# Optimization experiments

Measured on AMD Instinct MI355X. Metric: run time of the kernel, lower is better.

## Reference

```python
import jax, jax.numpy as jnp
import numpy as np
from jax import lax

B, N, H, W, C = 8, 1024, 256, 256, 256
HID = 512
RATES = (1, 3, 9, 9, 3, 1)


def setup_inputs() -> dict:
    key = jax.random.key(0)
    ks = jax.random.split(key, 16)
    # vertices are (row, col) float coordinates inside the feature map
    vertices = jax.random.uniform(ks[0], (B, N, 2), jnp.float32) * jnp.array([H - 1, W - 1], jnp.float32)
    features = jax.random.normal(ks[1], (B, H, W, C), jnp.float32)
    inp = {"vertices": vertices, "features": features}
    # Conv1D stack params (haiku Conv1D: kernel [K, Cin, Cout], bias [Cout])
    cin = C
    for i in range(6):
        inp[f"w{i}"] = jax.random.normal(ks[2 + 2 * i], (3, cin, HID), jnp.float32) * 0.05
        inp[f"b{i}"] = jax.random.normal(ks[3 + 2 * i], (HID,), jnp.float32) * 0.05
        cin = HID
    # offset head: Conv1D(2, 1, with_bias=False); original zero-init, randomized here
    inp["w_off"] = jax.random.normal(ks[14], (1, HID, 2), jnp.float32) * 0.05
    return inp


def _conv1d(x, w, b, rate):
    # x: [B, N, Cin], w: [K, Cin, Cout] -> SAME-padded dilated conv over vertex axis
    y = lax.conv_general_dilated(x, w, window_strides=(1,), padding="SAME",
                                 rhs_dilation=(rate,),
                                 dimension_numbers=("NWC", "WIO", "NWC"))
    return y if b is None else y + b


def _sample_at_vertices(vertices, features):
    # bilinear interpolation, zero outside (map_coordinates order=1 mode='constant')
    Bb, Hh, Ww, Cc = features.shape
    y, x = vertices[..., 0], vertices[..., 1]  # [B, N]
    y0f, x0f = jnp.floor(y), jnp.floor(x)
    wy1, wx1 = y - y0f, x - x0f
    wy0, wx0 = 1.0 - wy1, 1.0 - wx1
    y0, x0 = y0f.astype(jnp.int32), x0f.astype(jnp.int32)
    flat = features.reshape(Bb, Hh * Ww, Cc)

    def gather(yi, xi, wgt):
        valid = (yi >= 0) & (yi < Hh) & (xi >= 0) & (xi < Ww)
        idx = jnp.clip(yi, 0, Hh - 1) * Ww + jnp.clip(xi, 0, Ww - 1)  # [B, N]
        vals = jnp.take_along_axis(flat, idx[..., None], axis=1)  # [B, N, C]
        return vals * (wgt * valid)[..., None]

    return (gather(y0, x0, wy0 * wx0) + gather(y0, x0 + 1, wy0 * wx1)
            + gather(y0 + 1, x0, wy1 * wx0) + gather(y0 + 1, x0 + 1, wy1 * wx1))


def reference(vertices, features, w0, b0, w1, b1, w2, b2, w3, b3, w4, b4, w5, b5, w_off):
    h = _sample_at_vertices(vertices, features)  # [B, N, C]
    ws = (w0, w1, w2, w3, w4, w5)
    bs = (b0, b1, b2, b3, b4, b5)
    for w, b, r in zip(ws, bs, RATES):
        h = jax.nn.relu(_conv1d(h, w, b, r))
    offsets = _conv1d(h, w_off, None, 1)  # [B, N, 2]
    return vertices + offsets
```

## Files before the change

### kernel.cpp

```cpp
#include <hip/hip_runtime.h>

#define BATCH 8
#define NPTS  1024
#define FH    256
#define FW    256
#define FC    256
#define HID   512
#define PADN  1056
#define HALO  16

typedef __attribute__((ext_vector_type(8))) short short8;
typedef __attribute__((ext_vector_type(16))) float f32x16;
typedef unsigned short ushort_t;
typedef unsigned int uint_t;

__device__ __forceinline__ ushort_t f2bf(float f) {
    uint_t u = __builtin_bit_cast(uint_t, f);
    u += 0x7fffu + ((u >> 16) & 1u);
    return (ushort_t)(u >> 16);
}
__device__ __forceinline__ float bf2f(ushort_t s) {
    uint_t u = ((uint_t)s) << 16;
    return __builtin_bit_cast(float, u);
}

#define GLOAD16(g, l)                                                     \
    __builtin_amdgcn_global_load_lds(                                     \
        (const __attribute__((address_space(1))) void*)(g),               \
        (__attribute__((address_space(3))) void*)(l), 16, 0, 0)

__device__ __forceinline__ short8 gread16(const short* p) {
    short8 r;
    asm volatile("global_load_dwordx4 %0, %1, off" : "=v"(r) : "v"(p));
    return r;
}

__global__ __launch_bounds__(256) void prep_kernel(
    const float* __restrict__ vertices, const float* __restrict__ features,
    const float* __restrict__ w0, const float* __restrict__ w1,
    const float* __restrict__ w2, const float* __restrict__ w3,
    const float* __restrict__ w4, const float* __restrict__ w5,
    ushort_t* __restrict__ wt0, ushort_t* __restrict__ wt1,
    ushort_t* __restrict__ wt2, ushort_t* __restrict__ wt3,
    ushort_t* __restrict__ wt4, ushort_t* __restrict__ wt5,
    ushort_t* __restrict__ XpA, ushort_t* __restrict__ XpB,
    ushort_t* __restrict__ XpC, float* __restrict__ out)
{
    __shared__ float tile[64][65];
    const int blk = blockIdx.x;
    const int tid = threadIdx.x;

    if (blk < 1280) {
        int i = blk * 256 + tid;
        if (i < 65536) {
            int b = i >> 13, rem = i & 8191;
            int strip = rem >> 12, off = rem & 4095;
            XpA[(size_t)b * (PADN * FC) + (strip ? (PADN - HALO) * FC : 0) + off] = 0;
        }
        int jB = i - 65536;
        if (jB >= 0 && jB < 262144) {
            ushort_t* T = (jB < 131072) ? XpB : XpC;
            int j = jB & 131071;
            int b = j >> 14, rem = j & 16383;
            int strip = rem >> 13, off = rem & 8191;
            T[(size_t)b * (PADN * HID) + (strip ? (PADN - HALO) * HID : 0) + off] = 0;
        }
        return;
    }

    if (blk < 2336) {
        int j = blk - 1280;
        const float* w; ushort_t* wt; int CIN, kk0, co0;
        if (j < 96) {
            w = w0; wt = wt0; CIN = FC;
            kk0 = (j % 12) * 64; co0 = (j / 12) * 64;
        } else {
            int j2 = j - 96;
            int layer = j2 / 192, jj = j2 % 192;
            const float* ws[5]  = {w1, w2, w3, w4, w5};
            ushort_t*   wts[5]  = {wt1, wt2, wt3, wt4, wt5};
            w = ws[layer]; wt = wts[layer]; CIN = HID;
            kk0 = (jj % 24) * 64; co0 = (jj / 24) * 64;
        }
        int tap = kk0 / CIN, ci0 = kk0 - tap * CIN;
        int SL  = (3 * CIN) >> 4;
#pragma unroll 4
        for (int it = 0; it < 16; ++it) {
            int r = it * 4 + (tid >> 6);
            tile[r][tid & 63] = w[((size_t)tap * CIN + ci0 + r) * HID + co0 + (tid & 63)];
        }
        __syncthreads();
        int gl  = tid >> 7;
        int r2  = tid & 127;
        int l   = r2 >> 1;
        int j0  = (r2 & 1) * 4;
        int gco = (co0 >> 5) + gl;
        int kb  = ((l >> 5) << 3);
        int cl  = gl * 32 + (l & 31);
#pragma unroll
        for (int si = 0; si < 4; ++si) {
            int s = (kk0 >> 4) + si;
            ushort4 v;
            v.x = f2bf(tile[si * 16 + kb + j0 + 0][cl]);
            v.y = f2bf(tile[si * 16 + kb + j0 + 1][cl]);
            v.z = f2bf(tile[si * 16 + kb + j0 + 2][cl]);
            v.w = f2bf(tile[si * 16 + kb + j0 + 3][cl]);
            *(ushort4*)(wt + ((((size_t)gco * SL) + s) << 9) + l * 8 + j0) = v;
        }
        return;
    }

    if (blk < 4384) {
        int p = (blk - 2336) * 4 + (tid >> 6);
        int b = p >> 10;
        int n = p & 1023;
        int t = tid & 63;

        float y = vertices[2 * p + 0];
        float x = vertices[2 * p + 1];
        float y0f = floorf(y), x0f = floorf(x);
        float wy1 = y - y0f, wx1 = x - x0f;
        float wy0 = 1.f - wy1, wx0 = 1.f - wx1;
        int y0 = (int)y0f, x0 = (int)x0f;

        float4 acc = make_float4(0.f, 0.f, 0.f, 0.f);
        const float4* fbase = (const float4*)features + (size_t)b * FH * FW * (FC / 4);

#define CORNER(yi, xi, wgt) {                                                  \
        int yy = (yi), xx = (xi);                                              \
        float wv = ((yy >= 0) && (yy < FH) && (xx >= 0) && (xx < FW)) ? (wgt) : 0.f; \
        int yc = yy < 0 ? 0 : (yy > FH - 1 ? FH - 1 : yy);                     \
        int xc = xx < 0 ? 0 : (xx > FW - 1 ? FW - 1 : xx);                     \
        float4 v = fbase[((size_t)yc * FW + xc) * (FC / 4) + t];               \
        acc.x += v.x * wv; acc.y += v.y * wv; acc.z += v.z * wv; acc.w += v.w * wv; }

        CORNER(y0,     x0,     wy0 * wx0);
        CORNER(y0,     x0 + 1, wy0 * wx1);
        CORNER(y0 + 1, x0,     wy1 * wx0);
        CORNER(y0 + 1, x0 + 1, wy1 * wx1);
#undef CORNER

        ushort4 o;
        o.x = f2bf(acc.x); o.y = f2bf(acc.y); o.z = f2bf(acc.z); o.w = f2bf(acc.w);
        *(ushort4*)(XpA + ((size_t)b * PADN + HALO + n) * FC + 4 * t) = o;
        return;
    }

    {
        int i = (blk - 4384) * 256 + tid;
        out[i] = vertices[i];
    }
}

template <int CIN, bool HEAD>
__global__ __launch_bounds__(512, 2) void conv_mfma(
    const ushort_t* __restrict__ Xp,
    const ushort_t* __restrict__ Wf,
    const float* __restrict__ bias,
    ushort_t* __restrict__ Yp,
    int rate,
    const float* __restrict__ w_off,
    float* __restrict__ out)
{
    constexpr int NC  = CIN / 64;
    constexpr int SL3 = CIN / 16;
    constexpr int SL  = 3 * SL3;
    __shared__ short lds[2][18432];

    const int tid  = threadIdx.x;
    const int wid  = tid >> 6;
    const int lane = tid & 63;
    const int wm   = wid >> 2;
    const int wk   = wid & 3;

    const int h  = blockIdx.x;
    const int bm = (h & 7) * 4 + (h >> 6);
    const int bn = (h >> 3) & 7;
    const int batch = bm >> 2;
    const int n0    = (bm & 3) * 256;
    const int co0   = bn * 64;

    const short* Xbase = (const short*)Xp + ((size_t)batch * PADN + n0) * CIN;
    const short* Wbase = (const short*)Wf + lane * 8;

    auto stageA = [&](int buf, int c) {
        const short* Ag = Xbase + c * 64;
        short* ldsA = &lds[buf][0];
#pragma unroll
        for (int it = 0; it < 4; ++it) {
            int slot = it * 512 + wid * 64 + lane;
            int row  = slot >> 3;
            int chnk = (slot & 7) ^ (row & 7);
            GLOAD16(Ag + (size_t)row * CIN + chnk * 8,
                    ldsA + (size_t)(it * 512 + wid * 64) * 8);
        }
        if (wid < 4) {
            int slot = 2048 + wid * 64 + lane;
            int row  = slot >> 3;
            int chnk = (slot & 7) ^ (row & 7);
            GLOAD16(Ag + (size_t)row * CIN + chnk * 8,
                    ldsA + (size_t)(2048 + wid * 64) * 8);
        }
    };
    auto loadB = [&](short8* dst, int c) {
#pragma unroll
        for (int t = 0; t < 3; ++t)
#pragma unroll
            for (int j = 0; j < 2; ++j) {
                size_t gco = (size_t)(bn * 2 + j);
                size_t sl  = (size_t)(t * SL3 + c * 4 + wk);
                dst[t * 2 + j] = gread16(Wbase + ((gco * SL + sl) << 9));
            }
    };

    f32x16 acc[4][2];
    const int rowA0 = wm * 128 + (lane & 31);
    {
        float bv0 = (wk == 0) ? bias[co0 + (lane & 31)] : 0.f;
        float bv1 = (wk == 0) ? bias[co0 + 32 + (lane & 31)] : 0.f;
#pragma unroll
        for (int i = 0; i < 4; ++i)
#pragma unroll
            for (int r = 0; r < 16; ++r) { acc[i][0][r] = bv0; acc[i][1][r] = bv1; }
    }

    short8 B0[6], B1[6];
    stageA(0, 0);
    __builtin_amdgcn_sched_barrier(0);
    loadB(B0, 0);
    __builtin_amdgcn_sched_barrier(0);
    asm volatile("s_waitcnt vmcnt(6)" ::: "memory");
    __builtin_amdgcn_s_barrier();
    __builtin_amdgcn_sched_barrier(0);

    int cur = 0;
    auto kstep = [&](int c, short8* Bcur, short8* Bnxt) {
        if (c + 1 < NC) stageA(cur ^ 1, c + 1);
        __builtin_amdgcn_sched_barrier(0);

        if (c + 1 < NC) asm volatile("s_waitcnt vmcnt(4)" ::: "memory");
        else            asm volatile("s_waitcnt vmcnt(0)" ::: "memory");
        __builtin_amdgcn_sched_barrier(0);

        const short* As = &lds[cur][0];
        const int ch = wk * 2 + (lane >> 5);
        __builtin_amdgcn_s_setprio(1);
#pragma unroll
        for (int t = 0; t < 3; ++t) {
            const int shift = 16 + (t - 1) * rate;
#pragma unroll
            for (int i = 0; i < 4; ++i) {
                int rr = rowA0 + i * 32 + shift;
                short8 av = *(const short8*)(As + rr * 64 + ((ch ^ (rr & 7)) << 3));
                acc[i][0] = __builtin_amdgcn_mfma_f32_32x32x16_bf16(
                    av, Bcur[t * 2 + 0], acc[i][0], 0, 0, 0);
                acc[i][1] = __builtin_amdgcn_mfma_f32_32x32x16_bf16(
                    av, Bcur[t * 2 + 1], acc[i][1], 0, 0, 0);
            }
        }
        __builtin_amdgcn_s_setprio(0);
        __builtin_amdgcn_sched_barrier(0);

        if (c + 1 < NC) {
            loadB(Bnxt, c + 1);
            __builtin_amdgcn_sched_barrier(0);
            asm volatile("s_waitcnt vmcnt(6)" ::: "memory");
        }
        __builtin_amdgcn_s_barrier();
        cur ^= 1;
    };

    for (int c = 0; c < NC; c += 2) {
        kstep(c,     B0, B1);
        kstep(c + 1, B1, B0);
    }

    float* pf = (float*)&lds[0][0];
#pragma unroll
    for (int p = 1; p < 4; ++p) {
        if (wk == p) {
#pragma unroll
            for (int i = 0; i < 4; ++i)
#pragma unroll
                for (int j = 0; j < 2; ++j)
#pragma unroll
                    for (int r = 0; r < 16; ++r)
                        pf[wm * 8192 + ((i * 2 + j) * 16 + r) * 64 + lane] = acc[i][j][r];
        }
        __syncthreads();
        if (wk == 0) {
#pragma unroll
            for (int i = 0; i < 4; ++i)
#pragma unroll
                for (int j = 0; j < 2; ++j)
#pragma unroll
                    for (int r = 0; r < 16; ++r)
                        acc[i][j][r] += pf[wm * 8192 + ((i * 2 + j) * 16 + r) * 64 + lane];
        }
        __syncthreads();
    }

    if (wk == 0) {
        if (!HEAD) {
            ushort_t* Yb = Yp + ((size_t)batch * PADN + HALO + n0) * HID + co0;
#pragma unroll
            for (int i = 0; i < 4; ++i) {
#pragma unroll
                for (int r = 0; r < 16; ++r) {
                    int rrow = wm * 128 + i * 32 + (r & 3) + 8 * (r >> 2) + 4 * (lane >> 5);
#pragma unroll
                    for (int j = 0; j < 2; ++j) {
                        float v = acc[i][j][r];
                        v = v > 0.f ? v : 0.f;
                        Yb[(size_t)rrow * HID + j * 32 + (lane & 31)] = f2bf(v);
                    }
                }
            }
        } else {
            const int col = lane & 31;
            float w00 = w_off[(co0 + col) * 2 + 0];
            float w01 = w_off[(co0 + col) * 2 + 1];
            float w10 = w_off[(co0 + 32 + col) * 2 + 0];
            float w11 = w_off[(co0 + 32 + col) * 2 + 1];
#pragma unroll
            for (int i = 0; i < 4; ++i) {
#pragma unroll
                for (int r = 0; r < 16; ++r) {
                    float v0 = acc[i][0][r]; v0 = v0 > 0.f ? v0 : 0.f;
                    float v1 = acc[i][1][r]; v1 = v1 > 0.f ? v1 : 0.f;
                    float s0 = v0 * w00 + v1 * w10;
                    float s1 = v0 * w01 + v1 * w11;
#pragma unroll
                    for (int m = 16; m >= 1; m >>= 1) {
                        s0 += __shfl_xor(s0, m);
                        s1 += __shfl_xor(s1, m);
                    }
                    if (col == 0) {
                        int row = n0 + wm * 128 + i * 32 + (r & 3) + 8 * (r >> 2) + 4 * (lane >> 5);
                        float* op = out + 2 * ((size_t)batch * NPTS + row);
                        atomicAdd(op + 0, s0);
                        atomicAdd(op + 1, s1);
                    }
                }
            }
        }
    }
}

extern "C" void kernel_launch(void* const* d_in, const int* in_sizes, int n_in,
                              void* d_out, int out_size, void* d_ws, size_t ws_size,
                              hipStream_t stream)
{
    (void)in_sizes; (void)n_in; (void)out_size; (void)ws_size;

    const float* vertices = (const float*)d_in[0];
    const float* features = (const float*)d_in[1];
    const float* w[6]  = {(const float*)d_in[2], (const float*)d_in[4],
                          (const float*)d_in[6], (const float*)d_in[8],
                          (const float*)d_in[10], (const float*)d_in[12]};
    const float* bb[6] = {(const float*)d_in[3], (const float*)d_in[5],
                          (const float*)d_in[7], (const float*)d_in[9],
                          (const float*)d_in[11], (const float*)d_in[13]};
    const float* w_off = (const float*)d_in[14];
    float* out = (float*)d_out;

    char* p = (char*)d_ws;
    ushort_t* wt[6];
    wt[0] = (ushort_t*)p; p += (size_t)HID * (3 * FC) * 2;
    for (int i = 1; i < 6; ++i) { wt[i] = (ushort_t*)p; p += (size_t)HID * (3 * HID) * 2; }
    ushort_t* XpA = (ushort_t*)p; p += (size_t)BATCH * PADN * FC  * 2;
    ushort_t* XpB = (ushort_t*)p; p += (size_t)BATCH * PADN * HID * 2;
    ushort_t* XpC = (ushort_t*)p;

    prep_kernel<<<4448, 256, 0, stream>>>(
        vertices, features, w[0], w[1], w[2], w[3], w[4], w[5],
        wt[0], wt[1], wt[2], wt[3], wt[4], wt[5], XpA, XpB, XpC, out);

    static const int rates[6] = {1, 3, 9, 9, 3, 1};
    conv_mfma<FC, false><<<256, 512, 0, stream>>>(
        XpA, wt[0], bb[0], XpB, rates[0], nullptr, nullptr);
    ushort_t* src = XpB;
    ushort_t* dst = XpC;
    for (int i = 1; i < 5; ++i) {
        conv_mfma<HID, false><<<256, 512, 0, stream>>>(
            src, wt[i], bb[i], dst, rates[i], nullptr, nullptr);
        ushort_t* tmp = src; src = dst; dst = tmp;
    }
    conv_mfma<HID, true><<<256, 512, 0, stream>>>(
        src, wt[5], bb[5], dst, rates[5], w_off, out);
}
```

Baseline: 142.4 us.

## Split warps over output columns and K halves to shrink split-K reduction

Result: faster. 124.1 us (-12.9%).

```diff
diff --git a/kernel.cpp b/kernel.cpp
--- a/kernel.cpp
+++ b/kernel.cpp
@@ -171,7 +171,8 @@
     const int wid  = tid >> 6;
     const int lane = tid & 63;
     const int wm   = wid >> 2;
-    const int wk   = wid & 3;
+    const int wn   = (wid >> 1) & 1;
+    const int wk   = wid & 1;
 
     const int h  = blockIdx.x;
     const int bm = (h & 7) * 4 + (h >> 6);
@@ -181,7 +182,8 @@
     const int co0   = bn * 64;
 
     const short* Xbase = (const short*)Xp + ((size_t)batch * PADN + n0) * CIN;
-    const short* Wbase = (const short*)Wf + lane * 8;
+    const short* Wb = (const short*)Wf
+                    + (((size_t)(bn * 2 + wn) * SL) << 9) + lane * 8;
 
     auto stageA = [&](int buf, int c) {
         const short* Ag = Xbase + c * 64;
@@ -206,22 +208,20 @@
 #pragma unroll
         for (int t = 0; t < 3; ++t)
 #pragma unroll
-            for (int j = 0; j < 2; ++j) {
-                size_t gco = (size_t)(bn * 2 + j);
-                size_t sl  = (size_t)(t * SL3 + c * 4 + wk);
-                dst[t * 2 + j] = gread16(Wbase + ((gco * SL + sl) << 9));
-            }
+            for (int ksh = 0; ksh < 2; ++ksh)
+                dst[t * 2 + ksh] =
+                    gread16(Wb + ((size_t)(t * SL3 + c * 4 + wk * 2 + ksh) << 9));
     };
 
-    f32x16 acc[4][2];
+    f32x16 acc[4];
     const int rowA0 = wm * 128 + (lane & 31);
+    const int coB   = wn * 32 + (lane & 31);
     {
-        float bv0 = (wk == 0) ? bias[co0 + (lane & 31)] : 0.f;
-        float bv1 = (wk == 0) ? bias[co0 + 32 + (lane & 31)] : 0.f;
+        float bv = (wk == 0) ? bias[co0 + coB] : 0.f;
 #pragma unroll
         for (int i = 0; i < 4; ++i)
 #pragma unroll
-            for (int r = 0; r < 16; ++r) { acc[i][0][r] = bv0; acc[i][1][r] = bv1; }
+            for (int r = 0; r < 16; ++r) acc[i][r] = bv;
     }
 
     short8 B0[6], B1[6];
@@ -243,19 +243,20 @@
         __builtin_amdgcn_sched_barrier(0);
 
         const short* As = &lds[cur][0];
-        const int ch = wk * 2 + (lane >> 5);
         __builtin_amdgcn_s_setprio(1);
 #pragma unroll
         for (int t = 0; t < 3; ++t) {
             const int shift = 16 + (t - 1) * rate;
 #pragma unroll
-            for (int i = 0; i < 4; ++i) {
-                int rr = rowA0 + i * 32 + shift;
-                short8 av = *(const short8*)(As + rr * 64 + ((ch ^ (rr & 7)) << 3));
-                acc[i][0] = __builtin_amdgcn_mfma_f32_32x32x16_bf16(
-                    av, Bcur[t * 2 + 0], acc[i][0], 0, 0, 0);
-                acc[i][1] = __builtin_amdgcn_mfma_f32_32x32x16_bf16(
-                    av, Bcur[t * 2 + 1], acc[i][1], 0, 0, 0);
+            for (int ksh = 0; ksh < 2; ++ksh) {
+                int ch = (wk * 2 + ksh) * 2 + (lane >> 5);
+#pragma unroll
+                for (int i = 0; i < 4; ++i) {
+                    int rr = rowA0 + i * 32 + shift;
+                    short8 av = *(const short8*)(As + rr * 64 + ((ch ^ (rr & 7)) << 3));
+                    acc[i] = __builtin_amdgcn_mfma_f32_32x32x16_bf16(
+                        av, Bcur[t * 2 + ksh], acc[i], 0, 0, 0);
+                }
             }
         }
         __builtin_amdgcn_s_setprio(0);
@@ -276,30 +277,15 @@
     }
 
     float* pf = (float*)&lds[0][0];
-#pragma unroll
-    for (int p = 1; p < 4; ++p) {
-        if (wk == p) {
-#pragma unroll
-            for (int i = 0; i < 4; ++i)
-#pragma unroll
-                for (int j = 0; j < 2; ++j)
-#pragma unroll
-                    for (int r = 0; r < 16; ++r)
-                        pf[wm * 8192 + ((i * 2 + j) * 16 + r) * 64 + lane] = acc[i][j][r];
-        }
-        __syncthreads();
-        if (wk == 0) {
-#pragma unroll
-            for (int i = 0; i < 4; ++i)
-#pragma unroll
-                for (int j = 0; j < 2; ++j)
-#pragma unroll
-                    for (int r = 0; r < 16; ++r)
-                        acc[i][j][r] += pf[wm * 8192 + ((i * 2 + j) * 16 + r) * 64 + lane];
-        }
-        __syncthreads();
-    }
-
+    const int pair = wm * 2 + wn;
+    if (wk == 1) {
+#pragma unroll
+        for (int i = 0; i < 4; ++i)
+#pragma unroll
+            for (int r = 0; r < 16; ++r)
+                pf[pair * 4096 + (i * 16 + r) * 64 + lane] = acc[i][r];
+    }
+    __syncthreads();
     if (wk == 0) {
         if (!HEAD) {
             ushort_t* Yb = Yp + ((size_t)batch * PADN + HALO + n0) * HID + co0;
@@ -308,34 +294,28 @@
 #pragma unroll
                 for (int r = 0; r < 16; ++r) {
                     int rrow = wm * 128 + i * 32 + (r & 3) + 8 * (r >> 2) + 4 * (lane >> 5);
-#pragma unroll
-                    for (int j = 0; j < 2; ++j) {
-                        float v = acc[i][j][r];
-                        v = v > 0.f ? v : 0.f;
-                        Yb[(size_t)rrow * HID + j * 32 + (lane & 31)] = f2bf(v);
-                    }
+                    float v = acc[i][r] + pf[pair * 4096 + (i * 16 + r) * 64 + lane];
+                    v = v > 0.f ? v : 0.f;
+                    Yb[(size_t)rrow * HID + coB] = f2bf(v);
                 }
             }
         } else {
-            const int col = lane & 31;
-            float w00 = w_off[(co0 + col) * 2 + 0];
-            float w01 = w_off[(co0 + col) * 2 + 1];
-            float w10 = w_off[(co0 + 32 + col) * 2 + 0];
-            float w11 = w_off[(co0 + 32 + col) * 2 + 1];
+            float wc0 = w_off[(co0 + coB) * 2 + 0];
+            float wc1 = w_off[(co0 + coB) * 2 + 1];
 #pragma unroll
             for (int i = 0; i < 4; ++i) {
 #pragma unroll
                 for (int r = 0; r < 16; ++r) {
-                    float v0 = acc[i][0][r]; v0 = v0 > 0.f ? v0 : 0.f;
-                    float v1 = acc[i][1][r]; v1 = v1 > 0.f ? v1 : 0.f;
-                    float s0 = v0 * w00 + v1 * w10;
-                    float s1 = v0 * w01 + v1 * w11;
+                    float v = acc[i][r] + pf[pair * 4096 + (i * 16 + r) * 64 + lane];
+                    v = v > 0.f ? v : 0.f;
+                    float s0 = v * wc0;
+                    float s1 = v * wc1;
 #pragma unroll
                     for (int m = 16; m >= 1; m >>= 1) {
                         s0 += __shfl_xor(s0, m);
                         s1 += __shfl_xor(s1, m);
                     }
-                    if (col == 0) {
+                    if ((lane & 31) == 0) {
                         int row = n0 + wm * 128 + i * 32 + (r & 3) + 8 * (r >> 2) + 4 * (lane >> 5);
                         float* op = out + 2 * ((size_t)batch * NPTS + row);
                         atomicAdd(op + 0, s0);
```
